# Kernel tuning notes

Measured on AMD Instinct MI355X. Metric: run time of the kernel, lower is better.

The kernel has to match this reference:

```python
import jax, jax.numpy as jnp
import numpy as np

B = 2048          # query batch
DIM = 256         # embedding dim (first component timelike)
SLOTS = 65536     # memory slots, count N == SLOTS (full memory)
K_TOP = 32
SIM_THRESHOLD = 0.0
LOOP_EPS = 1e-3
DECAY = 0.99


def setup_inputs() -> dict:
    key = jax.random.key(0)
    k1, k2, k3 = jax.random.split(key, 3)
    q = jax.random.normal(k1, (B, DIM), dtype=jnp.float32)
    mem = jax.random.normal(k2, (SLOTS, DIM), dtype=jnp.float32)
    age = jax.random.uniform(k3, (SLOTS,), dtype=jnp.float32) * 50.0
    return {"q": q, "mem": mem, "age": age}


def _eigen_similarity(q, mem):
    # Lorentz-invariant (Minkowski) similarity, normalized to [-1, 1].
    # metric = diag(+1, -1, ..., -1): first component timelike.
    d = q.shape[-1]
    metric = jnp.concatenate([jnp.ones((1,), q.dtype), -jnp.ones((d - 1,), q.dtype)])
    inner = jnp.einsum('bd,nd->bn', q * metric, mem)              # (B, N)
    qn = jnp.sqrt(jnp.abs(jnp.sum(q * q * metric, axis=-1))) + 1e-6   # (B,)
    mn = jnp.sqrt(jnp.abs(jnp.sum(mem * mem * metric, axis=-1))) + 1e-6  # (N,)
    return jnp.clip(inner / (qn[:, None] * mn[None, :]), -1.0, 1.0)


def reference(q, mem, age):
    sim = _eigen_similarity(q, mem)                               # (B, N)
    # loop prevention: |sim| < eps treated as self/lightlike -> zeroed
    sim = jnp.where(jnp.abs(sim) < LOOP_EPS, jnp.zeros_like(sim), sim)
    # threshold mask: disconnected entries -> -inf
    sim = jnp.where(sim <= SIM_THRESHOLD, -jnp.inf, sim)
    # temporal decay as additive log-bias
    decay_factor = jnp.clip(DECAY ** age, 1e-6, None)             # (N,)
    sim = sim + jnp.log(decay_factor)[None, :]
    sim_topk, idx_topk = jax.lax.top_k(sim, K_TOP)                # (B, k) each
    attn = jax.nn.softmax(sim_topk, axis=-1)                      # (B, k)
    mem_topk = mem[idx_topk]                                      # (B, k, D) gather
    retrieved = jnp.einsum('bk,bkd->bd', attn, mem_topk)          # (B, D)
    return retrieved
```

## Files before the change

kernel.cpp:

```cpp
#include <hip/hip_runtime.h>
#include <hip/hip_bf16.h>
#include <math.h>

#define BQ 2048
#define DIM 256
#define SLOTS 65536
#define KTOP 32
#define CAP 256
#define LCAP 10
#define POOL 48
#define TAU0 0.11f

typedef __attribute__((ext_vector_type(8))) short short8;
typedef __attribute__((ext_vector_type(4))) float f32x4;
typedef unsigned long long u64;
typedef __attribute__((address_space(3))) const char* lds_cp;

__device__ inline unsigned mono(float f) {
    unsigned u = __float_as_uint(f);
    return u ^ ((0u - (u >> 31)) | 0x80000000u);
}

__device__ inline ushort f2bf(float x) {
    __hip_bfloat16 h = __float2bfloat16(x);
    return *(ushort*)&h;
}

__device__ __forceinline__ void gl2lds16(const void* g, void* l) {
    __builtin_amdgcn_global_load_lds((__attribute__((address_space(1))) void*)(void*)g,
                                     (__attribute__((address_space(3))) void*)l, 16, 0, 0);
}

__device__ __forceinline__ short8 dsr128(lds_cp p) {
    short8 d;
    asm volatile("ds_read_b128 %0, %1" : "=v"(d) : "v"(p));
    return d;
}

__global__ __launch_bounds__(256) void prep_mem_k(
    const float* __restrict__ mem, const float* __restrict__ age,
    ushort* __restrict__ mhat, float* __restrict__ mn, float* __restrict__ logdec,
    unsigned* __restrict__ counts)
{
    int t = threadIdx.x, lane = t & 63, w = t >> 6;
    if (blockIdx.x < BQ / 256) counts[blockIdx.x * 256 + t] = 0u;
    int slot = blockIdx.x * 4 + w;
    const float4* row = (const float4*)(mem + (size_t)slot * DIM);
    float4 v = row[lane];
    float p = -(v.x*v.x + v.y*v.y + v.z*v.z + v.w*v.w);
    if (lane == 0) p += 2.f * v.x * v.x;
    for (int m = 1; m < 64; m <<= 1) p += __shfl_xor(p, m);
    float nv = sqrtf(fabsf(p)) + 1e-6f;
    if (lane == 0) {
        mn[slot] = nv;
        float df = powf(0.99f, age[slot]);
        if (df < 1e-6f) df = 1e-6f;
        logdec[slot] = logf(df);
    }
    float inv = 1.f / nv;
    ushort4 o;
    o.x = f2bf(v.x * inv); o.y = f2bf(v.y * inv);
    o.z = f2bf(v.z * inv); o.w = f2bf(v.w * inv);
    *(ushort4*)&mhat[(size_t)slot * DIM + lane * 4] = o;
}

__global__ __launch_bounds__(256) void prep_q_k(
    const float* __restrict__ q, ushort* __restrict__ qhat, float* __restrict__ qs)
{
    int t = threadIdx.x, lane = t & 63, w = t >> 6;
    int b = blockIdx.x * 4 + w;
    const float4* row = (const float4*)(q + (size_t)b * DIM);
    float4 v = row[lane];
    float p = -(v.x*v.x + v.y*v.y + v.z*v.z + v.w*v.w);
    if (lane == 0) p += 2.f * v.x * v.x;
    for (int m = 1; m < 64; m <<= 1) p += __shfl_xor(p, m);
    float nv = sqrtf(fabsf(p)) + 1e-6f;
    float inv = 1.f / nv;
    float4 sv;
    sv.x = (lane == 0) ? v.x * inv : -v.x * inv;
    sv.y = -v.y * inv; sv.z = -v.z * inv; sv.w = -v.w * inv;
    *(float4*)&qs[(size_t)b * DIM + lane * 4] = sv;
    ushort4 o;
    o.x = f2bf(sv.x); o.y = f2bf(sv.y); o.z = f2bf(sv.z); o.w = f2bf(sv.w);
    *(ushort4*)&qhat[(size_t)b * DIM + lane * 4] = o;
}

__global__ __launch_bounds__(512, 2) void screen_k(
    const ushort* __restrict__ qhat, const ushort* __restrict__ mhat,
    const float* __restrict__ logdec,
    unsigned* __restrict__ counts, u64* __restrict__ cand)
{
    __shared__ __align__(16) short As[4][8192];
    __shared__ __align__(16) short Bs[4][8192];
    __shared__ float tauS[256];
    __shared__ unsigned lcount[256];
    __shared__ u64 lbuf[256 * LCAP];

    int t = threadIdx.x;
    int id = blockIdx.x;
    int xcd = id & 7, slotid = id >> 3;
    int rg = slotid & 7, cgl = slotid >> 3;
    int row0 = rg * 256;
    int col0 = (cgl * 8 + xcd) * 256;
    if (t < 256) { tauS[t] = TAU0 - logdec[col0 + t]; lcount[t] = 0u; }

    int lane = t & 63, w = t >> 6;
    int wm = w >> 2, wn = w & 3;
    int l15 = lane & 15, hi = lane >> 4;

    int r0 = t >> 2,         cl0 = t & 3;
    int r1 = (t + 512) >> 2, cl1 = (t + 512) & 3;
    const ushort* aSrc0 = qhat + (size_t)(row0 + r0) * DIM + (cl0 ^ ((r0 >> 1) & 3)) * 8;
    const ushort* aSrc1 = qhat + (size_t)(row0 + r1) * DIM + (cl1 ^ ((r1 >> 1) & 3)) * 8;
    const ushort* bSrc0 = mhat + (size_t)(col0 + r0) * DIM + (cl0 ^ ((r0 >> 1) & 3)) * 8;
    const ushort* bSrc1 = mhat + (size_t)(col0 + r1) * DIM + (cl1 ^ ((r1 >> 1) & 3)) * 8;
    int wb = w * 1024;

    f32x4 acc[8][4] = {};
    short8 af0[8], bf0[4], af1[8], bf1[4];

    #define STAGE(kt) do { \
        const int s_ = (kt) & 3; const int ke_ = (kt) * 32; \
        gl2lds16(aSrc0 + ke_, (char*)As[s_] + wb); \
        gl2lds16(aSrc1 + ke_, (char*)As[s_] + 8192 + wb); \
        gl2lds16(bSrc0 + ke_, (char*)Bs[s_] + wb); \
        gl2lds16(bSrc1 + ke_, (char*)Bs[s_] + 8192 + wb); \
    } while (0)

    int axk = (hi ^ ((l15 >> 1) & 3)) * 16;
    lds_cp aBase = (lds_cp)(const char*)&As[0][0] + (wm * 128 + l15) * 64 + axk;
    lds_cp bBase = (lds_cp)(const char*)&Bs[0][0] + (wn * 64 + l15) * 64 + axk;

    #define DSREAD(kt, AF, BF) do { \
        lds_cp a_ = aBase + ((kt) & 3) * 16384; \
        lds_cp b_ = bBase + ((kt) & 3) * 16384; \
        BF[0]=dsr128(b_);      BF[1]=dsr128(b_+1024); \
        BF[2]=dsr128(b_+2048); BF[3]=dsr128(b_+3072); \
        AF[0]=dsr128(a_);      AF[1]=dsr128(a_+1024); \
        AF[2]=dsr128(a_+2048); AF[3]=dsr128(a_+3072); \
        AF[4]=dsr128(a_+4096); AF[5]=dsr128(a_+5120); \
        AF[6]=dsr128(a_+6144); AF[7]=dsr128(a_+7168); \
    } while (0)

    #define MMA(AF, BF) do { \
        _Pragma("unroll") \
        for (int i_ = 0; i_ < 8; ++i_) { \
            _Pragma("unroll") \
            for (int j_ = 0; j_ < 4; ++j_) \
                acc[i_][j_] = __builtin_amdgcn_mfma_f32_16x16x32_bf16(AF[i_], BF[j_], acc[i_][j_], 0, 0, 0); \
        } \
    } while (0)

    STAGE(0); STAGE(1); STAGE(2); STAGE(3);
    asm volatile("s_waitcnt vmcnt(12)" ::: "memory");
    __builtin_amdgcn_s_barrier();
    DSREAD(0, af0, bf0);

    #define ITER(kt, CURA, CURB, NXTA, NXTB) do { \
        if ((kt) <= 4)      asm volatile("s_waitcnt vmcnt(8)" ::: "memory"); \
        else if ((kt) == 5) asm volatile("s_waitcnt vmcnt(4)" ::: "memory"); \
        else if ((kt) == 6) asm volatile("s_waitcnt vmcnt(0)" ::: "memory"); \
        asm volatile("s_waitcnt lgkmcnt(0)" ::: "memory");  \
        if ((kt) < 7) { \
            __builtin_amdgcn_s_barrier(); \
            if ((kt) <= 3) STAGE((kt) + 4); \
            DSREAD((kt) + 1, NXTA, NXTB); \
        } \
        __builtin_amdgcn_sched_barrier(0); \
        __builtin_amdgcn_s_setprio(1); \
        MMA(CURA, CURB); \
        __builtin_amdgcn_s_setprio(0); \
        __builtin_amdgcn_sched_barrier(0); \
    } while (0)

    ITER(0, af0, bf0, af1, bf1);
    ITER(1, af1, bf1, af0, bf0);
    ITER(2, af0, bf0, af1, bf1);
    ITER(3, af1, bf1, af0, bf0);
    ITER(4, af0, bf0, af1, bf1);
    ITER(5, af1, bf1, af0, bf0);
    ITER(6, af0, bf0, af1, bf1);
    ITER(7, af1, bf1, af0, bf0);

    #undef ITER
    #undef MMA
    #undef DSREAD
    #undef STAGE

    int rq = hi * 4;
    #pragma unroll
    for (int i = 0; i < 8; ++i)
        #pragma unroll
        for (int j = 0; j < 4; ++j) {
            int coll = wn * 64 + j * 16 + l15;
            float tau = tauS[coll];
            float ld = TAU0 - tau;
            #pragma unroll
            for (int g = 0; g < 4; ++g) {
                float sv = acc[i][j][g];
                if (sv > tau) {
                    int rloc = wm * 128 + i * 16 + rq + g;
                    unsigned p = atomicAdd(&lcount[rloc], 1u);
                    if (p < LCAP)
                        lbuf[rloc * LCAP + p] =
                            (((u64)mono(sv + ld)) << 32) | (unsigned)(col0 + coll);
                }
            }
        }
    __syncthreads();

    if (t < 256) {
        int n = (int)lcount[t]; if (n > LCAP) n = LCAP;
        if (n > 0) {
            unsigned base = atomicAdd(&counts[row0 + t], (unsigned)n);
            for (int k = 0; k < n; ++k) {
                unsigned pos = base + (unsigned)k;
                if (pos < CAP)
                    cand[(size_t)(row0 + t) * CAP + pos] = lbuf[t * LCAP + k];
            }
        }
    }
}

__global__ __launch_bounds__(256, 4) void rescore_finalize_k(
    const float* __restrict__ qs, const float* __restrict__ mem,
    const float* __restrict__ mn, const float* __restrict__ logdec,
    const unsigned* __restrict__ counts, const u64* __restrict__ cand,
    float* __restrict__ out)
{
    __shared__ __align__(16) float qsh[DIM];
    __shared__ u64 ckey[CAP];
    __shared__ int sidx[POOL];
    __shared__ float es[POOL];
    __shared__ u64 ek[POOL];
    __shared__ float aw[KTOP];
    __shared__ int aidx[KTOP];
    __shared__ float red4a[4], red4b[4];

    int b = blockIdx.x, t = threadIdx.x;
    int lane = t & 63, wv = t >> 6;
    int cnt = (int)counts[b];
    if (cnt > CAP) cnt = CAP;
    int T = cnt < POOL ? cnt : POOL;

    qsh[t] = qs[(size_t)b * DIM + t];
    if (t < KTOP) { aw[t] = 0.f; aidx[t] = 0; }
    if (t < cnt) {
        u64 raw = cand[(size_t)b * CAP + t];
        ckey[t] = raw ^ 0xFFFFFFFFull;
    }
    __syncthreads();

    if (t < cnt) {
        u64 mykey = ckey[t];
        int rank = 0;
        for (int j = 0; j < cnt; ++j) rank += (ckey[j] > mykey);
        if (rank < POOL) sidx[rank] = (int)(~(unsigned)(mykey & 0xFFFFFFFFull));
    }
    if (t >= T && t < POOL) { es[t] = -1e30f; ek[t] = 0ull; }
    __syncthreads();

    {
        const float4* q4 = (const float4*)qsh;
        float4 qv = q4[lane];
        for (int c = wv; c < T; c += 4) {
            int si = sidx[c];
            float4 mv = ((const float4*)(mem + (size_t)si * DIM))[lane];
            float part = qv.x*mv.x + qv.y*mv.y + qv.z*mv.z + qv.w*mv.w;
            #pragma unroll
            for (int m = 1; m < 64; m <<= 1) part += __shfl_xor(part, m);
            if (lane == 0) {
                float sim = part / mn[si];
                sim = fminf(fmaxf(sim, -1.f), 1.f);
                if (fabsf(sim) < 1e-3f) sim = 0.f;
                float sc = (sim > 0.f) ? sim + logdec[si] : -1e30f;
                es[c] = sc;
                ek[c] = (((u64)mono(sc)) << 32) | (unsigned)(~(unsigned)si);
            }
        }
    }
    __syncthreads();

    float msc = -1e30f; int midx = 0; int mrank = KTOP;
    if (t < POOL) {
        u64 mykey = ek[t];
        int rank = 0;
        #pragma unroll
        for (int j = 0; j < POOL; ++j) rank += (ek[j] > mykey);
        if (rank < KTOP && es[t] > -1e29f) {
            msc = es[t];
            midx = (int)(~(unsigned)(mykey & 0xFFFFFFFFull));
            mrank = rank;
        }
    }
    float lmax = msc;
    #pragma unroll
    for (int m = 1; m < 64; m <<= 1) lmax = fmaxf(lmax, __shfl_xor(lmax, m));
    if (lane == 0) red4a[wv] = lmax;
    __syncthreads();
    float ms = fmaxf(fmaxf(red4a[0], red4a[1]), fmaxf(red4a[2], red4a[3]));

    float e = (mrank < KTOP) ? expf(msc - ms) : 0.f;
    if (mrank < KTOP) { aw[mrank] = e; aidx[mrank] = midx; }
    float ps = e;
    #pragma unroll
    for (int m = 1; m < 64; m <<= 1) ps += __shfl_xor(ps, m);
    if (lane == 0) red4b[wv] = ps;
    __syncthreads();
    float S = red4b[0] + red4b[1] + red4b[2] + red4b[3];
    float invS = (S > 0.f) ? 1.f / S : 0.f;

    float o = 0.f;
    for (int r0 = 0; r0 < KTOP; r0 += 8) {
        float w8[8]; int i8[8];
        #pragma unroll
        for (int u = 0; u < 8; ++u) { w8[u] = aw[r0 + u]; i8[u] = aidx[r0 + u]; }
        float p8[8];
        #pragma unroll
        for (int u = 0; u < 8; ++u) p8[u] = mem[(size_t)i8[u] * DIM + t];
        #pragma unroll
        for (int u = 0; u < 8; ++u) o += w8[u] * p8[u];
    }
    out[(size_t)b * DIM + t] = o * invS;
}

extern "C" void kernel_launch(void* const* d_in, const int* in_sizes, int n_in,
                              void* d_out, int out_size, void* d_ws, size_t ws_size,
                              hipStream_t stream)
{
    const float* q   = (const float*)d_in[0];
    const float* mem = (const float*)d_in[1];
    const float* age = (const float*)d_in[2];
    float* out = (float*)d_out;

    char* ws = (char*)d_ws;
    size_t off = 0;
    auto alloc = [&](size_t bytes) { size_t o = off; off = (off + bytes + 255) & ~255UL; return o; };
    ushort*   mhat   = (ushort*)(ws + alloc((size_t)SLOTS * DIM * 2));
    ushort*   qhat   = (ushort*)(ws + alloc((size_t)BQ * DIM * 2));
    float*    qs     = (float*)(ws + alloc((size_t)BQ * DIM * 4));
    float*    mn     = (float*)(ws + alloc((size_t)SLOTS * 4));
    float*    logdec = (float*)(ws + alloc((size_t)SLOTS * 4));
    unsigned* counts = (unsigned*)(ws + alloc((size_t)BQ * 4));
    u64*      cand   = (u64*)(ws + alloc((size_t)BQ * CAP * 8));

    hipLaunchKernelGGL(prep_mem_k, dim3(SLOTS / 4), dim3(256), 0, stream,
                       mem, age, mhat, mn, logdec, counts);
    hipLaunchKernelGGL(prep_q_k, dim3(BQ / 4), dim3(256), 0, stream, q, qhat, qs);
    hipLaunchKernelGGL(screen_k, dim3((BQ / 256) * (SLOTS / 256)), dim3(512), 0, stream,
                       qhat, mhat, logdec, counts, cand);
    hipLaunchKernelGGL(rescore_finalize_k, dim3(BQ), dim3(256), 0, stream,
                       qs, mem, mn, logdec, counts, cand, out);
}
```

Before: 284.6 us.

## Split A-fragment loads into halves to cut register pressure in MFMA loop

The GEMM main loop now holds A fragments as two 4-wide halves instead of double-buffered 8-wide sets. It interleaves LDS reads of the second half with MFMAs on the first, and moves the vmcnt wait and barrier to mid-iteration. Second-row source pointers are replaced by a constant offset from the first. This frees VGPRs and aims to overlap LDS reads with MFMA work, but it adds an extra lgkmcnt wait per iteration and less prefetch depth for A.

```diff
diff --git a/kernel.cpp b/kernel.cpp
--- a/kernel.cpp
+++ b/kernel.cpp
@@ -108,83 +108,83 @@
     int wm = w >> 2, wn = w & 3;
     int l15 = lane & 15, hi = lane >> 4;
 
-    int r0 = t >> 2,         cl0 = t & 3;
-    int r1 = (t + 512) >> 2, cl1 = (t + 512) & 3;
+    int r0 = t >> 2, cl0 = t & 3;
     const ushort* aSrc0 = qhat + (size_t)(row0 + r0) * DIM + (cl0 ^ ((r0 >> 1) & 3)) * 8;
-    const ushort* aSrc1 = qhat + (size_t)(row0 + r1) * DIM + (cl1 ^ ((r1 >> 1) & 3)) * 8;
     const ushort* bSrc0 = mhat + (size_t)(col0 + r0) * DIM + (cl0 ^ ((r0 >> 1) & 3)) * 8;
-    const ushort* bSrc1 = mhat + (size_t)(col0 + r1) * DIM + (cl1 ^ ((r1 >> 1) & 3)) * 8;
     int wb = w * 1024;
 
     f32x4 acc[8][4] = {};
-    short8 af0[8], bf0[4], af1[8], bf1[4];
+    short8 afX[4], afY[4], bf0[4], bf1[4];
 
     #define STAGE(kt) do { \
         const int s_ = (kt) & 3; const int ke_ = (kt) * 32; \
         gl2lds16(aSrc0 + ke_, (char*)As[s_] + wb); \
-        gl2lds16(aSrc1 + ke_, (char*)As[s_] + 8192 + wb); \
+        gl2lds16(aSrc0 + 128 * DIM + ke_, (char*)As[s_] + 8192 + wb); \
         gl2lds16(bSrc0 + ke_, (char*)Bs[s_] + wb); \
-        gl2lds16(bSrc1 + ke_, (char*)Bs[s_] + 8192 + wb); \
+        gl2lds16(bSrc0 + 128 * DIM + ke_, (char*)Bs[s_] + 8192 + wb); \
     } while (0)
 
     int axk = (hi ^ ((l15 >> 1) & 3)) * 16;
     lds_cp aBase = (lds_cp)(const char*)&As[0][0] + (wm * 128 + l15) * 64 + axk;
     lds_cp bBase = (lds_cp)(const char*)&Bs[0][0] + (wn * 64 + l15) * 64 + axk;
 
-    #define DSREAD(kt, AF, BF) do { \
-        lds_cp a_ = aBase + ((kt) & 3) * 16384; \
+    #define DSREAD_B(kt, BF) do { \
         lds_cp b_ = bBase + ((kt) & 3) * 16384; \
         BF[0]=dsr128(b_);      BF[1]=dsr128(b_+1024); \
         BF[2]=dsr128(b_+2048); BF[3]=dsr128(b_+3072); \
+    } while (0)
+    #define DSREAD_A0(kt, AF) do { \
+        lds_cp a_ = aBase + ((kt) & 3) * 16384; \
         AF[0]=dsr128(a_);      AF[1]=dsr128(a_+1024); \
         AF[2]=dsr128(a_+2048); AF[3]=dsr128(a_+3072); \
-        AF[4]=dsr128(a_+4096); AF[5]=dsr128(a_+5120); \
-        AF[6]=dsr128(a_+6144); AF[7]=dsr128(a_+7168); \
-    } while (0)
-
-    #define MMA(AF, BF) do { \
+    } while (0)
+    #define DSREAD_A1(kt, AF) do { \
+        lds_cp a_ = aBase + ((kt) & 3) * 16384 + 4096; \
+        AF[0]=dsr128(a_);      AF[1]=dsr128(a_+1024); \
+        AF[2]=dsr128(a_+2048); AF[3]=dsr128(a_+3072); \
+    } while (0)
+
+    #define MMA4(AF, BF, I0) do { \
         _Pragma("unroll") \
-        for (int i_ = 0; i_ < 8; ++i_) { \
+        for (int i_ = 0; i_ < 4; ++i_) { \
             _Pragma("unroll") \
             for (int j_ = 0; j_ < 4; ++j_) \
-                acc[i_][j_] = __builtin_amdgcn_mfma_f32_16x16x32_bf16(AF[i_], BF[j_], acc[i_][j_], 0, 0, 0); \
+                acc[(I0)+i_][j_] = __builtin_amdgcn_mfma_f32_16x16x32_bf16(AF[i_], BF[j_], acc[(I0)+i_][j_], 0, 0, 0); \
         } \
     } while (0)
+
+    #define SB __builtin_amdgcn_sched_barrier(0)
 
     STAGE(0); STAGE(1); STAGE(2); STAGE(3);
     asm volatile("s_waitcnt vmcnt(12)" ::: "memory");
     __builtin_amdgcn_s_barrier();
-    DSREAD(0, af0, bf0);
-
-    #define ITER(kt, CURA, CURB, NXTA, NXTB) do { \
-        if ((kt) <= 4)      asm volatile("s_waitcnt vmcnt(8)" ::: "memory"); \
-        else if ((kt) == 5) asm volatile("s_waitcnt vmcnt(4)" ::: "memory"); \
-        else if ((kt) == 6) asm volatile("s_waitcnt vmcnt(0)" ::: "memory"); \
-        asm volatile("s_waitcnt lgkmcnt(0)" ::: "memory");  \
+    DSREAD_B(0, bf0); DSREAD_A0(0, afX); SB;
+
+    #define ITER(kt, BFC, BFN) do { \
+        asm volatile("s_waitcnt lgkmcnt(0)" ::: "memory"); SB;    \
+        DSREAD_A1(kt, afY); SB;                                   \
+        __builtin_amdgcn_s_setprio(1); MMA4(afX, BFC, 0); __builtin_amdgcn_s_setprio(0); SB; \
+        asm volatile("s_waitcnt lgkmcnt(0)" ::: "memory"); SB;    \
         if ((kt) < 7) { \
-            __builtin_amdgcn_s_barrier(); \
+            if ((kt) <= 4)      asm volatile("s_waitcnt vmcnt(8)" ::: "memory"); \
+            else if ((kt) == 5) asm volatile("s_waitcnt vmcnt(4)" ::: "memory"); \
+            else                asm volatile("s_waitcnt vmcnt(0)" ::: "memory"); \
+            __builtin_amdgcn_s_barrier();                         \
             if ((kt) <= 3) STAGE((kt) + 4); \
-            DSREAD((kt) + 1, NXTA, NXTB); \
+            DSREAD_B((kt)+1, BFN); DSREAD_A0((kt)+1, afX); SB;    \
         } \
-        __builtin_amdgcn_sched_barrier(0); \
-        __builtin_amdgcn_s_setprio(1); \
-        MMA(CURA, CURB); \
-        __builtin_amdgcn_s_setprio(0); \
-        __builtin_amdgcn_sched_barrier(0); \
-    } while (0)
-
-    ITER(0, af0, bf0, af1, bf1);
-    ITER(1, af1, bf1, af0, bf0);
-    ITER(2, af0, bf0, af1, bf1);
-    ITER(3, af1, bf1, af0, bf0);
-    ITER(4, af0, bf0, af1, bf1);
-    ITER(5, af1, bf1, af0, bf0);
-    ITER(6, af0, bf0, af1, bf1);
-    ITER(7, af1, bf1, af0, bf0);
+        __builtin_amdgcn_s_setprio(1); MMA4(afY, BFC, 4); __builtin_amdgcn_s_setprio(0); SB; \
+    } while (0)
+
+    ITER(0, bf0, bf1); ITER(1, bf1, bf0); ITER(2, bf0, bf1); ITER(3, bf1, bf0);
+    ITER(4, bf0, bf1); ITER(5, bf1, bf0); ITER(6, bf0, bf1); ITER(7, bf1, bf0);
 
     #undef ITER
-    #undef MMA
-    #undef DSREAD
+    #undef SB
+    #undef MMA4
+    #undef DSREAD_A1
+    #undef DSREAD_A0
+    #undef DSREAD_B
     #undef STAGE
 
     int rq = hi * 4;
```

Measured after the change: 235.2 us. 17.4% less time.
